# Optimization experiments

Hardware: AMD Instinct MI355X
Metric: run time of the kernel (lower is better)

Reference implementation:

```python
import jax, jax.numpy as jnp
import numpy as np

EMBEDDING_DIM = 128
NEG = -1000.0


def setup_inputs() -> dict:
    key = jax.random.key(0)
    ks = jax.random.split(key, 7)
    B, S_src, S_tgt, D = 2, 4096, 512, EMBEDDING_DIM
    return {
        "input_embeddings": jax.random.normal(ks[0], (B, S_src, D), dtype=jnp.float32),
        "token_attention_masks_source": jax.random.randint(ks[1], (B, S_src), 0, 2, dtype=jnp.int32),
        "token_attention_masks_target": jax.random.randint(ks[2], (B, S_tgt), 0, 2, dtype=jnp.int32),
        "encoder_output_embedding": jax.random.normal(ks[3], (B, S_tgt, D), dtype=jnp.float32),
        "w_query": jax.random.uniform(ks[4], (D, D), dtype=jnp.float32),
        "w_key": jax.random.uniform(ks[5], (D, D), dtype=jnp.float32),
        "w_value": jax.random.uniform(ks[6], (D, D), dtype=jnp.float32),
    }


def reference(input_embeddings, token_attention_masks_source,
              token_attention_masks_target, encoder_output_embedding,
              w_query, w_key, w_value):
    # Encoder self-attention branch (attention_type='encoder'), num_heads=1.
    D = w_query.shape[0]
    q = jnp.einsum('bsd,de->bse', input_embeddings, w_query)   # [B,S,D]
    k = jnp.einsum('bsd,de->bse', input_embeddings, w_key)     # [B,S,D]
    v = jnp.einsum('bsd,de->bse', input_embeddings, w_value)   # [B,S,D]
    scores = jnp.einsum('bsd,btd->bst', q, k) / jnp.sqrt(jnp.float32(D))
    # Original adds mask along the QUERY axis: mask[B,S] -> unsqueeze(-1).
    add_mask = jnp.where(token_attention_masks_source == 0, NEG, 0.0).astype(scores.dtype)
    scores = scores + add_mask[:, :, None]
    probs = jax.nn.softmax(scores, axis=2)                      # softmax over keys
    out = jnp.einsum('bst,btd->bsd', probs, v)                  # [B,S,D]
    return out
```

## Files before the change

kernel.cpp:

```cpp
#include <hip/hip_runtime.h>
#include <hip/hip_bf16.h>

#define S_SRC 4096
#define DIM 128
#define BATCH 2
#define NSP 8
#define NQB 32
#define NQG 512
#define NWIN 8

typedef unsigned short u16;
typedef unsigned int u32;
typedef __bf16 bf16x8 __attribute__((ext_vector_type(8)));
typedef float f32x4 __attribute__((ext_vector_type(4)));
typedef u32 u32x4 __attribute__((ext_vector_type(4)));
typedef u16 u16x8 __attribute__((ext_vector_type(8)));

__device__ __forceinline__ __bf16 bf_hi(float x) { return (__bf16)x; }
__device__ __forceinline__ __bf16 bf_lo(float x, __bf16 h) { return (__bf16)(x - (float)h); }
__device__ __forceinline__ u16 bfu(__bf16 h) { return __builtin_bit_cast(u16, h); }
__device__ __forceinline__ u16 f2bu(float x) { return __builtin_bit_cast(u16, (__bf16)x); }
__device__ __forceinline__ float bu2f(u16 u) { return (float)__builtin_bit_cast(__bf16, u); }
__device__ __forceinline__ u32 pk2(float lo, float hi) {
  return (u32)f2bu(lo) | ((u32)f2bu(hi) << 16);
}
__device__ __forceinline__ float ex2(float x) {
  float r;
  asm("v_exp_f32 %0, %1" : "=v"(r) : "v"(x));
  return r;
}
__device__ __forceinline__ void g2l16(const u16* src, u16* ldst) {
  __builtin_amdgcn_global_load_lds((const __attribute__((address_space(1))) void*)src,
                                   (__attribute__((address_space(3))) void*)ldst, 16, 0, 0);
}
#define MFMA __builtin_amdgcn_mfma_f32_16x16x32_bf16

__global__ __launch_bounds__(256) void k_wsplit(const float* __restrict__ wq,
                                                const float* __restrict__ wk,
                                                const float* __restrict__ wv,
                                                u16* __restrict__ wt) {
  int idx = blockIdx.x * 256 + threadIdx.x;
  int mat = idx >> 14;
  int r = idx & 16383;
  int d = r >> 7, e = r & 127;
  const float* w = (mat == 0) ? wq : ((mat == 1) ? wk : wv);
  float x = w[r];
  if (mat == 0) x *= 0.12751744684693238f;
  __bf16 h = bf_hi(x);
  __bf16 l = bf_lo(x, h);
  wt[((mat * 2 + 0) * 128 + e) * 128 + d] = bfu(h);
  wt[((mat * 2 + 1) * 128 + e) * 128 + d] = bfu(l);
}

__global__ __launch_bounds__(256) void k_proj(const float* __restrict__ X,
                                              const u16* __restrict__ wt,
                                              u16* __restrict__ Qh, u16* __restrict__ Ql,
                                              u16* __restrict__ Kh, u16* __restrict__ Kl,
                                              u16* __restrict__ VT) {
  const int b = blockIdx.x >> 7;
  const int tile = blockIdx.x & 127;
  const int tid = threadIdx.x;
  const int w = tid >> 6, lane = tid & 63, g = lane >> 4, l16 = lane & 15;

  bf16x8 a_h[2][4], a_l[2][4];
#pragma unroll
  for (int mf = 0; mf < 2; ++mf) {
    int row = tile * 32 + mf * 16 + l16;
    const float* xr = X + ((size_t)b * S_SRC + row) * DIM;
#pragma unroll
    for (int kf = 0; kf < 4; ++kf) {
      int d0 = kf * 32 + g * 8;
      f32x4 x0 = *(const f32x4*)(xr + d0);
      f32x4 x1 = *(const f32x4*)(xr + d0 + 4);
#pragma unroll
      for (int j = 0; j < 4; ++j) {
        __bf16 h0 = bf_hi(x0[j]);
        __bf16 h1 = bf_hi(x1[j]);
        a_h[mf][kf][j] = h0;
        a_l[mf][kf][j] = bf_lo(x0[j], h0);
        a_h[mf][kf][4 + j] = h1;
        a_l[mf][kf][4 + j] = bf_lo(x1[j], h1);
      }
    }
  }

#pragma unroll
  for (int mat = 0; mat < 3; ++mat) {
    const u16* wth = wt + (mat * 2 + 0) * 16384;
    const u16* wtl = wt + (mat * 2 + 1) * 16384;
#pragma unroll
    for (int nf = 0; nf < 2; ++nf) {
      int col = w * 32 + nf * 16 + l16;
      f32x4 acc[2];
      acc[0] = (f32x4){0.f, 0.f, 0.f, 0.f};
      acc[1] = (f32x4){0.f, 0.f, 0.f, 0.f};
#pragma unroll
      for (int kf = 0; kf < 4; ++kf) {
        int d0 = kf * 32 + g * 8;
        bf16x8 bh = *(const bf16x8*)(const void*)(wth + col * 128 + d0);
        bf16x8 bl = *(const bf16x8*)(const void*)(wtl + col * 128 + d0);
#pragma unroll
        for (int mf = 0; mf < 2; ++mf) {
          acc[mf] = MFMA(a_h[mf][kf], bh, acc[mf], 0, 0, 0);
          acc[mf] = MFMA(a_h[mf][kf], bl, acc[mf], 0, 0, 0);
          acc[mf] = MFMA(a_l[mf][kf], bh, acc[mf], 0, 0, 0);
        }
      }
#pragma unroll
      for (int mf = 0; mf < 2; ++mf)
#pragma unroll
        for (int r = 0; r < 4; ++r) {
          int row = tile * 32 + mf * 16 + g * 4 + r;
          float v = acc[mf][r];
          if (mat == 2) {
            VT[((size_t)b * DIM + col) * S_SRC + row] = f2bu(v);
          } else {
            __bf16 h = bf_hi(v);
            __bf16 l = bf_lo(v, h);
            size_t o = ((size_t)b * S_SRC + row) * DIM + col;
            if (mat == 0) { Qh[o] = bfu(h); Ql[o] = bfu(l); }
            else          { Kh[o] = bfu(h); Kl[o] = bfu(l); }
          }
        }
    }
  }
}

__global__ __launch_bounds__(512, 2) void k_attn(const u16* __restrict__ Qh, const u16* __restrict__ Ql,
                                                 const u16* __restrict__ Kh, const u16* __restrict__ Kl,
                                                 const u16* __restrict__ VT,
                                                 float* __restrict__ Pm, float* __restrict__ Pl,
                                                 u16* __restrict__ PO) {
  const int bid = blockIdx.x;
  const int sp = bid & 7;
  const int qb = bid >> 3;
  const int b = qb >> 4;
  const int tid = threadIdx.x;
  const int w = tid >> 6, lane = tid & 63, g = lane >> 4, l16 = lane & 15;

  __shared__ alignas(16) u16 kbuf[3][16384];
  __shared__ alignas(16) u16 vbuf[3][8192];

  const int gr0 = qb * 256 + w * 32;
  bf16x8 qh0[4], ql0[4], qh1[4], ql1[4];
  {
    const u16* p0h = Qh + ((size_t)gr0 + l16) * DIM;
    const u16* p0l = Ql + ((size_t)gr0 + l16) * DIM;
    const u16* p1h = Qh + ((size_t)gr0 + 16 + l16) * DIM;
    const u16* p1l = Ql + ((size_t)gr0 + 16 + l16) * DIM;
#pragma unroll
    for (int kf = 0; kf < 4; ++kf) {
      int d0 = kf * 32 + g * 8;
      qh0[kf] = *(const bf16x8*)(const void*)(p0h + d0);
      ql0[kf] = *(const bf16x8*)(const void*)(p0l + d0);
      qh1[kf] = *(const bf16x8*)(const void*)(p1h + d0);
      ql1[kf] = *(const bf16x8*)(const void*)(p1l + d0);
    }
  }

  f32x4 acc0[8], acc1[8];
#pragma unroll
  for (int nf = 0; nf < 8; ++nf) {
    acc0[nf] = (f32x4){0.f, 0.f, 0.f, 0.f};
    acc1[nf] = (f32x4){0.f, 0.f, 0.f, 0.f};
  }
  float m0 = -1e30f, m1 = -1e30f, l0 = 0.f, l1 = 0.f;

  const int key_base = sp * (S_SRC / NSP);
  const u16* KhB = Kh + (size_t)b * S_SRC * DIM;
  const u16* KlB = Kl + (size_t)b * S_SRC * DIM;
  const u16* VTB = VT + (size_t)b * DIM * S_SRC;

  const int kkey0 = tid >> 4;
  const int kks = ((tid & 15) ^ (kkey0 & 15)) << 3;
  const int vd0 = tid >> 3;
  const int vks = ((tid & 7) ^ ((vd0 >> 1) & 7)) << 3;
  const int wb = w * 512;
  const int mg = ((g & 1) << 1) | (g >> 1);

#define STAGE(BUF, KEY0)                                                             \
  {                                                                                  \
    g2l16(KhB + ((size_t)((KEY0) + kkey0)) * DIM + kks,      &kbuf[BUF][wb]);        \
    g2l16(KhB + ((size_t)((KEY0) + 32 + kkey0)) * DIM + kks, &kbuf[BUF][4096 + wb]); \
    g2l16(KlB + ((size_t)((KEY0) + kkey0)) * DIM + kks,      &kbuf[BUF][8192 + wb]); \
    g2l16(KlB + ((size_t)((KEY0) + 32 + kkey0)) * DIM + kks, &kbuf[BUF][12288 + wb]);\
    g2l16(VTB + (size_t)vd0 * S_SRC + (KEY0) + vks,          &vbuf[BUF][wb]);        \
    g2l16(VTB + (size_t)(64 + vd0) * S_SRC + (KEY0) + vks,   &vbuf[BUF][4096 + wb]); \
  }

#define SMPACK(S, MR, LR, ACC, PA, PB)                                               \
  {                                                                                  \
    float mxa = fmaxf(fmaxf(fmaxf(S[0][0], S[0][1]), fmaxf(S[0][2], S[0][3])),       \
                      fmaxf(fmaxf(S[1][0], S[1][1]), fmaxf(S[1][2], S[1][3])));      \
    float mxb = fmaxf(fmaxf(fmaxf(S[2][0], S[2][1]), fmaxf(S[2][2], S[2][3])),       \
                      fmaxf(fmaxf(S[3][0], S[3][1]), fmaxf(S[3][2], S[3][3])));      \
    float mx = fmaxf(mxa, mxb);                                                      \
    mx = fmaxf(mx, __shfl_xor(mx, 16, 64));                                          \
    mx = fmaxf(mx, __shfl_xor(mx, 32, 64));                                          \
    if (!__all(mx - MR <= 11.5f)) {                                                  \
      float mn = fmaxf(MR, mx);                                                      \
      float f = ex2(MR - mn);                                                        \
      LR *= f; MR = mn;                                                              \
      float fr0 = __shfl(f, g * 4 + 0, 64);                                          \
      float fr1 = __shfl(f, g * 4 + 1, 64);                                          \
      float fr2 = __shfl(f, g * 4 + 2, 64);                                          \
      float fr3 = __shfl(f, g * 4 + 3, 64);                                          \
      _Pragma("unroll")                                                              \
      for (int nf = 0; nf < 8; ++nf) {                                               \
        ACC[nf][0] *= fr0; ACC[nf][1] *= fr1;                                        \
        ACC[nf][2] *= fr2; ACC[nf][3] *= fr3;                                        \
      }                                                                              \
    }                                                                                \
    float e0 = ex2(S[0][0] - MR), e1 = ex2(S[0][1] - MR);                            \
    float e2 = ex2(S[0][2] - MR), e3 = ex2(S[0][3] - MR);                            \
    float e4 = ex2(S[1][0] - MR), e5 = ex2(S[1][1] - MR);                            \
    float e6 = ex2(S[1][2] - MR), e7 = ex2(S[1][3] - MR);                            \
    float f0 = ex2(S[2][0] - MR), f1 = ex2(S[2][1] - MR);                            \
    float f2 = ex2(S[2][2] - MR), f3 = ex2(S[2][3] - MR);                            \
    float f4 = ex2(S[3][0] - MR), f5 = ex2(S[3][1] - MR);                            \
    float f6 = ex2(S[3][2] - MR), f7 = ex2(S[3][3] - MR);                            \
    float sm = (((e0 + e1) + (e2 + e3)) + ((e4 + e5) + (e6 + e7)))                   \
             + (((f0 + f1) + (f2 + f3)) + ((f4 + f5) + (f6 + f7)));                  \
    sm += __shfl_xor(sm, 16, 64);                                                    \
    sm += __shfl_xor(sm, 32, 64);                                                    \
    LR += sm;                                                                        \
    bool odd = (g & 1);                                                              \
    {                                                                                \
      u32 w0 = pk2(e0, e1), w1 = pk2(e2, e3), w2 = pk2(e4, e5), w3 = pk2(e6, e7);    \
      u32 x0 = __shfl_xor(w0, 16, 64), x1 = __shfl_xor(w1, 16, 64);                  \
      u32 x2 = __shfl_xor(w2, 16, 64), x3 = __shfl_xor(w3, 16, 64);                  \
      u32x4 pw;                                                                      \
      pw.x = odd ? x2 : w0; pw.y = odd ? x3 : w1;                                    \
      pw.z = odd ? w2 : x0; pw.w = odd ? w3 : x1;                                    \
      PA = __builtin_bit_cast(bf16x8, pw);                                           \
    }                                                                                \
    {                                                                                \
      u32 w0 = pk2(f0, f1), w1 = pk2(f2, f3), w2 = pk2(f4, f5), w3 = pk2(f6, f7);    \
      u32 x0 = __shfl_xor(w0, 16, 64), x1 = __shfl_xor(w1, 16, 64);                  \
      u32 x2 = __shfl_xor(w2, 16, 64), x3 = __shfl_xor(w3, 16, 64);                  \
      u32x4 pw;                                                                      \
      pw.x = odd ? x2 : w0; pw.y = odd ? x3 : w1;                                    \
      pw.z = odd ? w2 : x0; pw.w = odd ? w3 : x1;                                    \
      PB = __builtin_bit_cast(bf16x8, pw);                                           \
    }                                                                                \
  }

  STAGE(0, key_base)
  STAGE(1, key_base + 64)

  int cur = 0;
  for (int i = 0; i < NWIN; ++i) {
    if (i < NWIN - 1) {
      asm volatile("s_waitcnt vmcnt(6)" ::: "memory");
    } else {
      asm volatile("s_waitcnt vmcnt(0)" ::: "memory");
    }
    __builtin_amdgcn_s_barrier();
    if (i + 2 < NWIN) {
      int nx = cur + 2; nx = (nx >= 3) ? nx - 3 : nx;
      STAGE(nx, key_base + (i + 2) * 64)
    }

    const u16* kb = kbuf[cur];
    const u16* vb = vbuf[cur];

    f32x4 sg0[4], sg1[4];
#pragma unroll
    for (int st = 0; st < 4; ++st) {
      sg0[st] = (f32x4){0.f, 0.f, 0.f, 0.f};
      sg1[st] = (f32x4){0.f, 0.f, 0.f, 0.f};
    }
    __builtin_amdgcn_s_setprio(1);
#pragma unroll
    for (int kf = 0; kf < 4; ++kf) {
      int cs = ((kf * 4 + g) ^ l16) << 3;
#pragma unroll
      for (int st = 0; st < 4; ++st) {
        const u16* kp = kb + (st * 16 + l16) * 128 + cs;
        bf16x8 kh = *(const bf16x8*)(const void*)kp;
        bf16x8 kl = *(const bf16x8*)(const void*)(kp + 8192);
        sg0[st] = MFMA(kh, qh0[kf], sg0[st], 0, 0, 0);
        sg0[st] = MFMA(kh, ql0[kf], sg0[st], 0, 0, 0);
        sg0[st] = MFMA(kl, qh0[kf], sg0[st], 0, 0, 0);
        sg1[st] = MFMA(kh, qh1[kf], sg1[st], 0, 0, 0);
        sg1[st] = MFMA(kh, ql1[kf], sg1[st], 0, 0, 0);
        sg1[st] = MFMA(kl, qh1[kf], sg1[st], 0, 0, 0);
      }
    }
    __builtin_amdgcn_s_setprio(0);

    bf16x8 pa0A, pa0B, pa1A, pa1B;
    SMPACK(sg0, m0, l0, acc0, pa0A, pa0B)
    SMPACK(sg1, m1, l1, acc1, pa1A, pa1B)

    __builtin_amdgcn_s_setprio(1);
#pragma unroll
    for (int nf = 0; nf < 8; ++nf) {
      int d = nf * 16 + l16;
      int sw = (d >> 1) & 7;
      const u16* vr = vb + d * 64;
      bf16x8 vf0 = *(const bf16x8*)(const void*)(vr + ((mg ^ sw) << 3));
      bf16x8 vf1 = *(const bf16x8*)(const void*)(vr + (((4 + mg) ^ sw) << 3));
      acc0[nf] = MFMA(pa0A, vf0, acc0[nf], 0, 0, 0);
      acc0[nf] = MFMA(pa0B, vf1, acc0[nf], 0, 0, 0);
      acc1[nf] = MFMA(pa1A, vf0, acc1[nf], 0, 0, 0);
      acc1[nf] = MFMA(pa1B, vf1, acc1[nf], 0, 0, 0);
    }
    __builtin_amdgcn_s_setprio(0);

    cur = (cur + 1 >= 3) ? cur - 2 : cur + 1;
  }

  const int pidx0 = sp * NQG + (gr0 >> 4);
  {
    u16* po = PO + (size_t)pidx0 * 16 * DIM;
#pragma unroll
    for (int nf = 0; nf < 8; ++nf)
#pragma unroll
      for (int r = 0; r < 4; ++r)
        po[(g * 4 + r) * DIM + nf * 16 + l16] = f2bu(acc0[nf][r]);
    u16* po1 = PO + (size_t)(pidx0 + 1) * 16 * DIM;
#pragma unroll
    for (int nf = 0; nf < 8; ++nf)
#pragma unroll
      for (int r = 0; r < 4; ++r)
        po1[(g * 4 + r) * DIM + nf * 16 + l16] = f2bu(acc1[nf][r]);
  }
  if (g == 0) { Pm[pidx0 * 16 + l16] = m0; Pl[pidx0 * 16 + l16] = l0; }
  if (g == 1) { Pm[(pidx0 + 1) * 16 + l16] = m1; Pl[(pidx0 + 1) * 16 + l16] = l1; }
#undef STAGE
#undef SMPACK
}

__global__ __launch_bounds__(256) void k_comb(const float* __restrict__ Pm,
                                              const float* __restrict__ Pl,
                                              const u16* __restrict__ PO,
                                              float* __restrict__ out) {
  const int qg = blockIdx.x;
  const int tid = threadIdx.x;

  __shared__ float sc[NSP][16];
  if (tid < 16) {
    float m = -1e30f;
#pragma unroll
    for (int s = 0; s < NSP; ++s) m = fmaxf(m, Pm[(s * NQG + qg) * 16 + tid]);
    float den = 0.f;
#pragma unroll
    for (int s = 0; s < NSP; ++s) {
      float e = exp2f(Pm[(s * NQG + qg) * 16 + tid] - m);
      sc[s][tid] = e;
      den += Pl[(s * NQG + qg) * 16 + tid] * e;
    }
    float inv = 1.0f / den;
#pragma unroll
    for (int s = 0; s < NSP; ++s) sc[s][tid] *= inv;
  }
  __syncthreads();

  const int e0 = tid * 8;
  const int row = e0 >> 7;
  float a[8];
#pragma unroll
  for (int j = 0; j < 8; ++j) a[j] = 0.f;
#pragma unroll
  for (int s = 0; s < NSP; ++s) {
    u16x8 p = *(const u16x8*)(const void*)(PO + (size_t)(s * NQG + qg) * 16 * DIM + e0);
    float wgt = sc[s][row];
#pragma unroll
    for (int j = 0; j < 8; ++j) a[j] += bu2f(p[j]) * wgt;
  }
  float* op = out + (size_t)qg * 16 * DIM + e0;
  f32x4 o0 = {a[0], a[1], a[2], a[3]};
  f32x4 o1 = {a[4], a[5], a[6], a[7]};
  *(f32x4*)op = o0;
  *(f32x4*)(op + 4) = o1;
}

extern "C" void kernel_launch(void* const* d_in, const int* in_sizes, int n_in,
                              void* d_out, int out_size, void* d_ws, size_t ws_size,
                              hipStream_t stream) {
  const float* X  = (const float*)d_in[0];
  const float* wq = (const float*)d_in[4];
  const float* wk = (const float*)d_in[5];
  const float* wv = (const float*)d_in[6];
  float* out = (float*)d_out;

  u16* WT = (u16*)d_ws;
  u16* Qh = WT + 3 * 2 * 128 * 128;
  u16* Ql = Qh + (size_t)BATCH * S_SRC * DIM;
  u16* Kh = Ql + (size_t)BATCH * S_SRC * DIM;
  u16* Kl = Kh + (size_t)BATCH * S_SRC * DIM;
  u16* VT = Kl + (size_t)BATCH * S_SRC * DIM;
  float* Pm = (float*)(VT + (size_t)BATCH * S_SRC * DIM);
  float* Pl = Pm + (size_t)NSP * NQG * 16;
  u16* PO = (u16*)(Pl + (size_t)NSP * NQG * 16);

  hipLaunchKernelGGL(k_wsplit, dim3(192), dim3(256), 0, stream, wq, wk, wv, WT);
  hipLaunchKernelGGL(k_proj, dim3(BATCH * S_SRC / 32), dim3(256), 0, stream,
                     X, WT, Qh, Ql, Kh, Kl, VT);
  hipLaunchKernelGGL(k_attn, dim3(NQB * NSP), dim3(512), 0, stream,
                     Qh, Ql, Kh, Kl, VT, Pm, Pl, PO);
  hipLaunchKernelGGL(k_comb, dim3(NQG), dim3(256), 0, stream, Pm, Pl, PO, out);
}
```

Baseline: 67.96 us.

## Fuse split-K combine into attention kernel via last-block atomic ticket

Removes the separate combine kernel launch by having the last of the eight key-split blocks for each query block (found with an atomic counter plus thread fences) merge the partial max, sum and outputs and write the final result. This saves a kernel launch and its tail, but adds a memset launch, an atomic and fences per block, extra shared memory for the scale table, and a serial combine tail done by only 32 blocks.

```diff
diff --git a/kernel.cpp b/kernel.cpp
--- a/kernel.cpp
+++ b/kernel.cpp
@@ -130,7 +130,8 @@
                                                  const u16* __restrict__ Kh, const u16* __restrict__ Kl,
                                                  const u16* __restrict__ VT,
                                                  float* __restrict__ Pm, float* __restrict__ Pl,
-                                                 u16* __restrict__ PO) {
+                                                 u16* __restrict__ PO, int* __restrict__ cnt,
+                                                 float* __restrict__ out) {
   const int bid = blockIdx.x;
   const int sp = bid & 7;
   const int qb = bid >> 3;
@@ -140,6 +141,8 @@
 
   __shared__ alignas(16) u16 kbuf[3][16384];
   __shared__ alignas(16) u16 vbuf[3][8192];
+  __shared__ float scl[NSP][256];
+  __shared__ int ticket;
 
   const int gr0 = qb * 256 + w * 32;
   bf16x8 qh0[4], ql0[4], qh1[4], ql1[4];
@@ -328,52 +331,57 @@
   }
   if (g == 0) { Pm[pidx0 * 16 + l16] = m0; Pl[pidx0 * 16 + l16] = l0; }
   if (g == 1) { Pm[(pidx0 + 1) * 16 + l16] = m1; Pl[(pidx0 + 1) * 16 + l16] = l1; }
+
+  __threadfence();
+  if (tid == 0) ticket = atomicAdd(&cnt[qb], 1);
+  __syncthreads();
+  if (ticket != NSP - 1) return;
+  __threadfence();
+
+  if (tid < 256) {
+    const int qg = qb * 16 + (tid >> 4);
+    const int rr = tid & 15;
+    float m = -1e30f;
+#pragma unroll
+    for (int s = 0; s < NSP; ++s) m = fmaxf(m, Pm[(s * NQG + qg) * 16 + rr]);
+    float den = 0.f;
+    float e[NSP];
+#pragma unroll
+    for (int s = 0; s < NSP; ++s) {
+      e[s] = ex2(Pm[(s * NQG + qg) * 16 + rr] - m);
+      den += Pl[(s * NQG + qg) * 16 + rr] * e[s];
+    }
+    float inv = 1.0f / den;
+#pragma unroll
+    for (int s = 0; s < NSP; ++s) scl[s][tid] = e[s] * inv;
+  }
+  __syncthreads();
+
+#pragma unroll
+  for (int it = 0; it < 8; ++it) {
+    const int idx = it * 4096 + tid * 8;
+    const int row = idx >> 7;
+    const int qg = qb * 16 + (row >> 4);
+    const int rl = row & 15;
+    const int col = idx & 127;
+    float a[8];
+#pragma unroll
+    for (int j = 0; j < 8; ++j) a[j] = 0.f;
+#pragma unroll
+    for (int s = 0; s < NSP; ++s) {
+      u16x8 p = *(const u16x8*)(const void*)(PO + ((size_t)((s * NQG + qg) * 16 + rl)) * DIM + col);
+      float wgt = scl[s][row];
+#pragma unroll
+      for (int j = 0; j < 8; ++j) a[j] += bu2f(p[j]) * wgt;
+    }
+    float* op = out + ((size_t)qb * 256 + row) * DIM + col;
+    f32x4 o0 = {a[0], a[1], a[2], a[3]};
+    f32x4 o1 = {a[4], a[5], a[6], a[7]};
+    *(f32x4*)op = o0;
+    *(f32x4*)(op + 4) = o1;
+  }
 #undef STAGE
 #undef SMPACK
-}
-
-__global__ __launch_bounds__(256) void k_comb(const float* __restrict__ Pm,
-                                              const float* __restrict__ Pl,
-                                              const u16* __restrict__ PO,
-                                              float* __restrict__ out) {
-  const int qg = blockIdx.x;
-  const int tid = threadIdx.x;
-
-  __shared__ float sc[NSP][16];
-  if (tid < 16) {
-    float m = -1e30f;
-#pragma unroll
-    for (int s = 0; s < NSP; ++s) m = fmaxf(m, Pm[(s * NQG + qg) * 16 + tid]);
-    float den = 0.f;
-#pragma unroll
-    for (int s = 0; s < NSP; ++s) {
-      float e = exp2f(Pm[(s * NQG + qg) * 16 + tid] - m);
-      sc[s][tid] = e;
-      den += Pl[(s * NQG + qg) * 16 + tid] * e;
-    }
-    float inv = 1.0f / den;
-#pragma unroll
-    for (int s = 0; s < NSP; ++s) sc[s][tid] *= inv;
-  }
-  __syncthreads();
-
-  const int e0 = tid * 8;
-  const int row = e0 >> 7;
-  float a[8];
-#pragma unroll
-  for (int j = 0; j < 8; ++j) a[j] = 0.f;
-#pragma unroll
-  for (int s = 0; s < NSP; ++s) {
-    u16x8 p = *(const u16x8*)(const void*)(PO + (size_t)(s * NQG + qg) * 16 * DIM + e0);
-    float wgt = sc[s][row];
-#pragma unroll
-    for (int j = 0; j < 8; ++j) a[j] += bu2f(p[j]) * wgt;
-  }
-  float* op = out + (size_t)qg * 16 * DIM + e0;
-  f32x4 o0 = {a[0], a[1], a[2], a[3]};
-  f32x4 o1 = {a[4], a[5], a[6], a[7]};
-  *(f32x4*)op = o0;
-  *(f32x4*)(op + 4) = o1;
 }
 
 extern "C" void kernel_launch(void* const* d_in, const int* in_sizes, int n_in,
@@ -394,11 +402,12 @@
   float* Pm = (float*)(VT + (size_t)BATCH * S_SRC * DIM);
   float* Pl = Pm + (size_t)NSP * NQG * 16;
   u16* PO = (u16*)(Pl + (size_t)NSP * NQG * 16);
-
+  int* cnt = (int*)(PO + (size_t)NSP * NQG * 16 * DIM);
+
+  hipMemsetAsync(cnt, 0, NQB * sizeof(int), stream);
   hipLaunchKernelGGL(k_wsplit, dim3(192), dim3(256), 0, stream, wq, wk, wv, WT);
   hipLaunchKernelGGL(k_proj, dim3(BATCH * S_SRC / 32), dim3(256), 0, stream,
                      X, WT, Qh, Ql, Kh, Kl, VT);
   hipLaunchKernelGGL(k_attn, dim3(NQB * NSP), dim3(512), 0, stream,
-                     Qh, Ql, Kh, Kl, VT, Pm, Pl, PO);
-  hipLaunchKernelGGL(k_comb, dim3(NQG), dim3(256), 0, stream, Pm, Pl, PO, out);
-}
+                     Qh, Ql, Kh, Kl, VT, Pm, Pl, PO, cnt, out);
+}
```

New measurement: 153.8 us. 2.26x slower.
